# Kernel optimization log

Measured on AMD Instinct MI355X. Metric: run time of the kernel, lower is better.

Reference implementation:

```python
import jax, jax.numpy as jnp
import numpy as np

DIM = 784
HEADS = 2
DH = DIM // HEADS  # 392
EPS_LN = 1e-5
EPS_L2 = 1e-12


def layer_norm(x, w, b):
    mu = jnp.mean(x, axis=-1, keepdims=True)
    var = jnp.mean(jnp.square(x - mu), axis=-1, keepdims=True)
    return (x - mu) * jax.lax.rsqrt(var + EPS_LN) * w + b


def hardswish(x):
    return x * jnp.clip(x + 3.0, 0.0, 6.0) / 6.0


def l2norm(x):
    n = jnp.sqrt(jnp.sum(jnp.square(x), axis=-1, keepdims=True))
    return x / jnp.maximum(n, EPS_L2)


def setup_inputs() -> dict:
    key = jax.random.key(0)
    ks = jax.random.split(key, 8)
    B, N = 32, 1024
    x = jax.random.normal(ks[0], (B, N, DIM), dtype=jnp.float32)
    s = 0.02
    qkv_w = jax.random.normal(ks[1], (3 * DIM, DIM), dtype=jnp.float32) * s
    qkv_b = jax.random.normal(ks[2], (3 * DIM,), dtype=jnp.float32) * s
    out_w = jax.random.normal(ks[3], (DIM, DIM), dtype=jnp.float32) * s
    out_b = jax.random.normal(ks[4], (DIM,), dtype=jnp.float32) * s
    ffn_w = jax.random.normal(ks[5], (DIM, DIM), dtype=jnp.float32) * s
    ffn_b = jax.random.normal(ks[6], (DIM,), dtype=jnp.float32) * s
    ln_w = jnp.ones((DIM,), dtype=jnp.float32)
    ln_b = jnp.zeros((DIM,), dtype=jnp.float32)
    scale = jnp.ones((HEADS, 1, 1), dtype=jnp.float32) * 0.01
    return {"x": x, "ln_w": ln_w, "ln_b": ln_b, "qkv_w": qkv_w, "qkv_b": qkv_b,
            "scale": scale, "out_w": out_w, "out_b": out_b, "ffn_w": ffn_w, "ffn_b": ffn_b}


def reference(x, ln_w, ln_b, qkv_w, qkv_b, scale, out_w, out_b, ffn_w, ffn_b):
    B, N, _ = x.shape
    h = HEADS
    xn = layer_norm(x, ln_w, ln_b)
    qkv = xn @ qkv_w.T + qkv_b  # [B, N, 3*DIM]
    q, k, v = jnp.split(qkv, 3, axis=-1)
    # 'b n (h d) -> b h n d'
    def to_heads(t):
        return t.reshape(B, N, h, DH).transpose(0, 2, 1, 3)
    q, k, v = to_heads(q), to_heads(k), to_heads(v)
    q, k = l2norm(q), l2norm(k)
    sim = jnp.einsum('bhnd,bhmd->bhnm', q, k) * jnp.sqrt(scale)  # scale [h,1,1] broadcasts
    attn = jax.nn.softmax(sim, axis=-1)
    out = jnp.einsum('bhnm,bhmd->bhnd', attn, v)
    out = out.transpose(0, 2, 1, 3).reshape(B, N, DIM)  # 'b h n d -> b n (h d)'
    out = layer_norm(out, ln_w, ln_b)  # same LayerNorm params reused
    out = hardswish(out)
    out_ffn = hardswish(out @ ffn_w.T + ffn_b)
    return (out + out_ffn) @ out_w.T + out_b
```

## Files before the change

kernel.cpp:

```cpp
#include <hip/hip_runtime.h>

typedef unsigned short u16;
typedef unsigned int u32;
typedef __attribute__((ext_vector_type(4))) float f32x4;
typedef __attribute__((ext_vector_type(8))) short bf16x8;

#define TOK 32768
#define KP  832
#define DHP 448
#define DHPV 512
#define NQKV 2560

static __device__ __forceinline__ float bf2f(u16 u){ u32 v = ((u32)u)<<16; return __builtin_bit_cast(float, v); }
static __device__ __forceinline__ u16 f2bf(float f){
  u32 x = __builtin_bit_cast(u32, f);
  u32 r = (x + 0x7fffu + ((x>>16)&1u)) >> 16;
  return (u16)r;
}
static __device__ __forceinline__ void gload16(const void* g, void* l){
  __builtin_amdgcn_global_load_lds((const __attribute__((address_space(1))) void*)g,
                                   (__attribute__((address_space(3))) void*)l, 16, 0, 0);
}
static __device__ __forceinline__ float wave_red_sum(float v){
  #pragma unroll
  for (int o = 32; o > 0; o >>= 1) v += __shfl_xor(v, o, 64);
  return v;
}

__global__ __launch_bounds__(256) void wconv_k(const float* __restrict__ src, u16* __restrict__ dst,
                                               int srcR, long long total){
  long long i = (long long)blockIdx.x*256 + threadIdx.x;
  if (i >= total) return;
  int r = (int)(i / KP), c = (int)(i % KP);
  float v = (r < srcR && c < 784) ? src[(long long)r*784 + c] : 0.f;
  dst[i] = f2bf(v);
}

__global__ __launch_bounds__(256) void ln1_k(const float* __restrict__ x, const float* __restrict__ w,
                                             const float* __restrict__ b, u16* __restrict__ out){
  const int tid = threadIdx.x;
  const long long row = blockIdx.x;
  const float* xr = x + row*784;
  float v[4]; float s = 0.f, ss = 0.f;
  #pragma unroll
  for (int i = 0; i < 4; i++){ int c = tid + i*256; float t = (c < 784) ? xr[c] : 0.f; v[i] = t; s += t; ss += t*t; }
  __shared__ float red[8];
  s = wave_red_sum(s); ss = wave_red_sum(ss);
  if ((tid & 63) == 0){ red[tid>>6] = s; red[4 + (tid>>6)] = ss; }
  __syncthreads();
  float S  = red[0]+red[1]+red[2]+red[3];
  float SS = red[4]+red[5]+red[6]+red[7];
  float mean = S * (1.f/784.f);
  float var  = SS * (1.f/784.f) - mean*mean;
  float rstd = rsqrtf(var + 1e-5f);
  u16* orow = out + row*KP;
  #pragma unroll
  for (int i = 0; i < 4; i++){
    int c = tid + i*256;
    if (c < KP){
      u16 o = 0;
      if (c < 784) o = f2bf((v[i]-mean)*rstd*w[c] + b[c]);
      orow[c] = o;
    }
  }
}

__global__ __launch_bounds__(256) void ln2hs_k(const u16* __restrict__ a, const float* __restrict__ w,
                                               const float* __restrict__ b, u16* __restrict__ out){
  const int tid = threadIdx.x;
  const long long row = blockIdx.x;
  const u16* ar = a + row*784;
  float v[4]; float s = 0.f, ss = 0.f;
  #pragma unroll
  for (int i = 0; i < 4; i++){ int c = tid + i*256; float t = (c < 784) ? bf2f(ar[c]) : 0.f; v[i] = t; s += t; ss += t*t; }
  __shared__ float red[8];
  s = wave_red_sum(s); ss = wave_red_sum(ss);
  if ((tid & 63) == 0){ red[tid>>6] = s; red[4 + (tid>>6)] = ss; }
  __syncthreads();
  float S  = red[0]+red[1]+red[2]+red[3];
  float SS = red[4]+red[5]+red[6]+red[7];
  float mean = S * (1.f/784.f);
  float var  = SS * (1.f/784.f) - mean*mean;
  float rstd = rsqrtf(var + 1e-5f);
  u16* orow = out + row*KP;
  #pragma unroll
  for (int i = 0; i < 4; i++){
    int c = tid + i*256;
    if (c < KP){
      u16 o = 0;
      if (c < 784){
        float y = (v[i]-mean)*rstd*w[c] + b[c];
        y = y * fminf(fmaxf(y + 3.f, 0.f), 6.f) * (1.f/6.f);
        o = f2bf(y);
      }
      orow[c] = o;
    }
  }
}

__global__ __launch_bounds__(256) void l2n_k(u16* __restrict__ Q, u16* __restrict__ Kb,
                                             const float* __restrict__ scale){
  const int lane = threadIdx.x & 63, wv = threadIdx.x >> 6;
  const long long rid = (long long)blockIdx.x*4 + wv;
  const bool isK = rid >= 65536;
  const long long idx = isK ? rid - 65536 : rid;
  u16* base = (isK ? Kb : Q) + idx*DHP;
  uint2 t0 = *(const uint2*)(base + lane*4);
  int ch1 = lane + 64;
  uint2 t1 = (ch1 < 112) ? *(const uint2*)(base + ch1*4) : make_uint2(0u,0u);
  float f0[4], f1[4];
  u32 c0[2] = {t0.x, t0.y}, c1[2] = {t1.x, t1.y};
  #pragma unroll
  for (int j = 0; j < 4; j++){
    f0[j] = bf2f((u16)(c0[j>>1] >> ((j&1)*16)));
    f1[j] = bf2f((u16)(c1[j>>1] >> ((j&1)*16)));
  }
  float ssq = 0.f;
  #pragma unroll
  for (int j = 0; j < 4; j++) ssq += f0[j]*f0[j];
  if (ch1 < 98){
    #pragma unroll
    for (int j = 0; j < 4; j++) ssq += f1[j]*f1[j];
  }
  ssq = wave_red_sum(ssq);
  float fac = 1.f / fmaxf(sqrtf(ssq), 1e-12f);
  if (!isK) fac *= sqrtf(scale[(int)((idx >> 10) & 1)]);
  u32 o0[2], o1[2];
  #pragma unroll
  for (int j = 0; j < 2; j++){
    u16 lo = f2bf(f0[2*j]*fac),   hi = f2bf(f0[2*j+1]*fac);
    o0[j] = (u32)lo | ((u32)hi << 16);
    u16 lo1 = (ch1 < 98) ? f2bf(f1[2*j]*fac)   : (u16)0;
    u16 hi1 = (ch1 < 98) ? f2bf(f1[2*j+1]*fac) : (u16)0;
    o1[j] = (u32)lo1 | ((u32)hi1 << 16);
  }
  *(uint2*)(base + lane*4) = make_uint2(o0[0], o0[1]);
  if (ch1 < 112) *(uint2*)(base + ch1*4) = make_uint2(o1[0], o1[1]);
}

__global__ __launch_bounds__(512, 2) void attn_k(const u16* __restrict__ Qb, const u16* __restrict__ Kb,
    const u16* __restrict__ Vtb, u16* __restrict__ att)
{
  __shared__ u16 smem[32768];
  u16* Pbuf = smem + 16384;

  const int tid = threadIdx.x, lane = tid & 63, wid = tid >> 6;
  const int wq  = wid >> 2, kvw = wid & 3;
  const int dw  = wid >> 2, qw  = wid & 3;

  const int lin = (int)blockIdx.x;
  const int bh = (lin & 7)*8 + (lin >> 6);
  const int qt = (lin >> 3) & 7;

  const u16* Qp = Qb  + ((long long)bh*1024 + (long long)qt*128)*DHP;
  const u16* Kp = Kb  + (long long)bh*1024*DHP;
  const u16* Vp = Vtb + (long long)bh*DHPV*1024;

  const int srow = tid >> 2;
  const int scol = (((tid & 3) ^ ((srow >> 1) & 3)) << 3);
  const int s2   = tid + 512;
  const int r2   = s2 >> 2;
  const int c2   = (((s2 & 3) ^ ((r2 >> 1) & 3)) << 3);

  int offq[4], offk[2], offv[7];
  #pragma unroll
  for (int m = 0; m < 4; m++){
    int r = wq*64 + m*16 + (lane & 15);
    offq[m] = r*32 + ((((lane>>4) ^ (r>>1)) & 3) << 3);
  }
  #pragma unroll
  for (int n = 0; n < 2; n++){
    int r = kvw*32 + n*16 + (lane & 15);
    offk[n] = 4096 + r*32 + ((((lane>>4) ^ (r>>1)) & 3) << 3);
  }
  #pragma unroll
  for (int m = 0; m < 7; m++){
    int r = dw*112 + m*16 + (lane & 15);
    offv[m] = r*32 + ((((lane>>4) ^ (r>>1)) & 3) << 3);
  }

  auto stageA = [&](int ck, int t, int buf){
    u16* rb = smem + buf*8192;
    gload16(Qp + (long long)srow*DHP + t*32 + scol,            rb + tid*8);
    gload16(Kp + (long long)(ck*128 + srow)*DHP + t*32 + scol, rb + 4096 + tid*8);
  };
  auto stageV = [&](int ck, int ms, int buf){
    u16* rb = smem + buf*8192;
    const int h = ms >> 2, s = ms & 3;
    const u16* src = Vp + (long long)(h*224)*1024 + ck*128 + s*32;
    gload16(src + (long long)srow*1024 + scol, rb + tid*8);
    gload16(src + (long long)r2*1024  + c2,   rb + s2*8);
  };

  f32x4 oacc[2][7][2];
  #pragma unroll
  for (int h = 0; h < 2; h++)
    #pragma unroll
    for (int m = 0; m < 7; m++)
      #pragma unroll
      for (int n = 0; n < 2; n++) oacc[h][m][n] = f32x4{0.f,0.f,0.f,0.f};
  float rs_r[16];
  #pragma unroll
  for (int i = 0; i < 16; i++) rs_r[i] = 0.f;

  for (int ck = 0; ck < 8; ++ck){
    stageA(ck, 0, 0); stageA(ck, 1, 1);
    asm volatile("s_waitcnt vmcnt(2)" ::: "memory");
    __builtin_amdgcn_s_barrier();
    f32x4 sacc[4][2];
    #pragma unroll
    for (int m = 0; m < 4; m++)
      #pragma unroll
      for (int n = 0; n < 2; n++) sacc[m][n] = f32x4{0.f,0.f,0.f,0.f};

    for (int t = 0; t < 14; ++t){
      if (t + 2 < 14) stageA(ck, t+2, (t+2)%3);
      const u16* ra = smem + (t%3)*8192;
      bf16x8 aq[4], bk[2];
      #pragma unroll
      for (int m = 0; m < 4; m++) aq[m] = *(const bf16x8*)(ra + offq[m]);
      #pragma unroll
      for (int n = 0; n < 2; n++) bk[n] = *(const bf16x8*)(ra + offk[n]);
      __builtin_amdgcn_s_setprio(1);
      #pragma unroll
      for (int m = 0; m < 4; m++)
        #pragma unroll
        for (int n = 0; n < 2; n++)
          sacc[m][n] = __builtin_amdgcn_mfma_f32_16x16x32_bf16(aq[m], bk[n], sacc[m][n], 0, 0, 0);
      __builtin_amdgcn_s_setprio(0);
      if (t + 2 < 14)      asm volatile("s_waitcnt vmcnt(2)" ::: "memory");
      else if (t + 1 < 14) asm volatile("s_waitcnt vmcnt(0)" ::: "memory");
      if (t + 1 < 14) __builtin_amdgcn_s_barrier();
    }
    __builtin_amdgcn_s_barrier();

    stageV(ck, 0, 0);
    #pragma unroll
    for (int m = 0; m < 4; m++){
      #pragma unroll
      for (int i = 0; i < 4; i++){
        const int q = wq*64 + m*16 + (lane>>4)*4 + i;
        float a = 0.f;
        #pragma unroll
        for (int n = 0; n < 2; n++){
          const int kv = kvw*32 + n*16 + (lane & 15);
          u16 pb = f2bf(__expf(sacc[m][n][i]));
          Pbuf[q*128 + (((kv>>3) ^ (q&15)) << 3) + (kv&7)] = pb;
          a += bf2f(pb);
        }
        rs_r[m*4+i] += a;
      }
    }
    asm volatile("s_waitcnt vmcnt(0) lgkmcnt(0)" ::: "memory");
    __builtin_amdgcn_s_barrier();

    #pragma unroll
    for (int ms = 0; ms < 8; ++ms){
      if (ms + 1 < 8) stageV(ck, ms+1, (ms+1)&1);
      const u16* vb = smem + (ms&1)*8192;
      const int s = ms & 3;
      const int h = ms >> 2;
      bf16x8 av[7], bp[2];
      #pragma unroll
      for (int m = 0; m < 7; m++) av[m] = *(const bf16x8*)(vb + offv[m]);
      #pragma unroll
      for (int n = 0; n < 2; n++){
        const int q = qw*32 + n*16 + (lane & 15);
        const int cc = s*4 + (lane>>4);
        bp[n] = *(const bf16x8*)(Pbuf + q*128 + ((cc ^ (q&15)) << 3));
      }
      __builtin_amdgcn_s_setprio(1);
      #pragma unroll
      for (int m = 0; m < 7; m++)
        #pragma unroll
        for (int n = 0; n < 2; n++)
          oacc[h][m][n] = __builtin_amdgcn_mfma_f32_16x16x32_bf16(av[m], bp[n], oacc[h][m][n], 0, 0, 0);
      __builtin_amdgcn_s_setprio(0);
      if (ms + 1 < 8){
        asm volatile("s_waitcnt vmcnt(0)" ::: "memory");
        __builtin_amdgcn_s_barrier();
      }
    }
    __builtin_amdgcn_s_barrier();
  }

  float* rsL = (float*)&smem[0];
  float* rsT = rsL + 512;
  #pragma unroll
  for (int m = 0; m < 4; m++){
    #pragma unroll
    for (int i = 0; i < 4; i++){
      float v = rs_r[m*4+i];
      v += __shfl_xor(v, 1, 64); v += __shfl_xor(v, 2, 64);
      v += __shfl_xor(v, 4, 64); v += __shfl_xor(v, 8, 64);
      if ((lane & 15) == 0) rsL[(wq*64 + m*16 + (lane>>4)*4 + i)*4 + kvw] = v;
    }
  }
  __syncthreads();
  if (tid < 128) rsT[tid] = 1.f/(rsL[tid*4]+rsL[tid*4+1]+rsL[tid*4+2]+rsL[tid*4+3]);
  __syncthreads();
  const int b = bh >> 1, hh = bh & 1;
  #pragma unroll
  for (int h = 0; h < 2; h++){
    #pragma unroll
    for (int n = 0; n < 2; n++){
      const int q = qw*32 + n*16 + (lane & 15);
      const float rinv = rsT[q];
      u16* arw = att + ((long long)(b*1024 + qt*128 + q))*784 + hh*392;
      #pragma unroll
      for (int m = 0; m < 7; m++){
        const int d0 = h*224 + dw*112 + m*16 + (lane>>4)*4;
        if (d0 < 392){
          u16 a0 = f2bf(oacc[h][m][n][0]*rinv), a1 = f2bf(oacc[h][m][n][1]*rinv);
          u16 a2 = f2bf(oacc[h][m][n][2]*rinv), a3 = f2bf(oacc[h][m][n][3]*rinv);
          *(u32*)(arw + d0)     = (u32)a0 | ((u32)a1 << 16);
          *(u32*)(arw + d0 + 2) = (u32)a2 | ((u32)a3 << 16);
        }
      }
    }
  }
}

template<int EPI, int ORDER>
__global__ __launch_bounds__(512, 2) void gemm_k(const u16* __restrict__ Ab, const u16* __restrict__ Bb,
    int lda, int ldb, int nkt, long long sA, long long sB,
    const float* __restrict__ fp0, void* __restrict__ vp1, void* __restrict__ vp2, void* __restrict__ vp3)
{
  __shared__ u16 LA[3][8192];
  __shared__ u16 LB[3][4096];
  const int tid = threadIdx.x;
  const int lane = tid & 63;
  const int wid = tid >> 6;
  const int wr = wid >> 1, wc = wid & 1;

  const int gx = gridDim.x, gy = gridDim.y;
  const int nwg = gx*gy;
  int lin = (ORDER == 0) ? ((int)blockIdx.x + gx*(int)blockIdx.y)
                         : ((int)blockIdx.y + gy*(int)blockIdx.x);
  const int q8 = nwg >> 3, r8 = nwg & 7;
  const int xcd = lin & 7, base8 = lin >> 3;
  int wg = (xcd < r8 ? xcd*(q8+1) : r8*(q8+1) + (xcd-r8)*q8) + base8;
  int bx, by;
  if (ORDER == 0){ bx = wg % gx; by = wg / gx; }
  else           { by = wg % gy; bx = wg / gy; }

  const u16* A  = Ab + (long long)by*256*lda;
  const u16* Bp = Bb + (long long)bx*128*ldb;

  const int s0 = tid, s1 = tid + 512;
  const int r0 = s0 >> 2, r1 = s1 >> 2;
  const int kc0 = (((s0 & 3) ^ ((s0 >> 3) & 3)) << 3);
  const int kc1 = (((s1 & 3) ^ ((s1 >> 3) & 3)) << 3);
  const u16* ga0 = A  + (long long)r0*lda + kc0;
  const u16* ga1 = A  + (long long)r1*lda + kc1;
  const u16* gb0 = Bp + (long long)r0*ldb + kc0;

  int offa[4], offb[4];
  #pragma unroll
  for (int m = 0; m < 4; m++){
    int row = wr*64 + m*16 + (lane & 15);
    offa[m] = row*32 + ((((lane >> 4) ^ (row >> 1)) & 3) << 3);
  }
  #pragma unroll
  for (int n = 0; n < 4; n++){
    int row = wc*64 + n*16 + (lane & 15);
    offb[n] = row*32 + ((((lane >> 4) ^ (row >> 1)) & 3) << 3);
  }

  f32x4 acc[4][4];
  #pragma unroll
  for (int m = 0; m < 4; m++)
    #pragma unroll
    for (int n = 0; n < 4; n++) acc[m][n] = f32x4{0.f,0.f,0.f,0.f};

  auto stage = [&](int tt){
    const int b = tt % 3;
    const long long k0 = (long long)(tt << 5);
    gload16(ga0 + k0, (void*)&LA[b][s0*8]);
    gload16(ga1 + k0, (void*)&LA[b][s1*8]);
    gload16(gb0 + k0, (void*)&LB[b][tid*8]);
  };

  stage(0); stage(1);
  asm volatile("s_waitcnt vmcnt(3)" ::: "memory");
  __builtin_amdgcn_s_barrier();

  for (int t = 0; t < nkt; ++t){
    if (t + 2 < nkt) stage(t + 2);
    const int b = t % 3;
    bf16x8 af[4], bf[4];
    #pragma unroll
    for (int m = 0; m < 4; m++) af[m] = *(const bf16x8*)&LA[b][offa[m]];
    #pragma unroll
    for (int n = 0; n < 4; n++) bf[n] = *(const bf16x8*)&LB[b][offb[n]];
    __builtin_amdgcn_s_setprio(1);
    #pragma unroll
    for (int m = 0; m < 4; m++)
      #pragma unroll
      for (int n = 0; n < 4; n++)
        acc[m][n] = __builtin_amdgcn_mfma_f32_16x16x32_bf16(af[m], bf[n], acc[m][n], 0, 0, 0);
    __builtin_amdgcn_s_setprio(0);
    if (t + 2 < nkt)      asm volatile("s_waitcnt vmcnt(3)" ::: "memory");
    else if (t + 1 < nkt) asm volatile("s_waitcnt vmcnt(0)" ::: "memory");
    if (t + 1 < nkt) __builtin_amdgcn_s_barrier();
  }

  const int tm = by*256 + wr*64;
  const int tn = bx*128 + wc*64;

  if constexpr (EPI == 0){
    u16* Qn = (u16*)vp1; u16* Kn = (u16*)vp2; u16* Vt = (u16*)vp3;
    #pragma unroll
    for (int m = 0; m < 4; m++){
      const int row0 = tm + m*16 + (lane>>4)*4;
      if (row0 < 2352){
        const int seg = row0 / 392;
        const int hh = seg & 1;
        const int dd0 = row0 - seg*392;
        const float b0 = fp0[row0], b1 = fp0[row0+1], b2 = fp0[row0+2], b3 = fp0[row0+3];
        #pragma unroll
        for (int n = 0; n < 4; n++){
          const int col = tn + n*16 + (lane&15);
          const int bb = col >> 10, nn = col & 1023;
          if (seg < 4){
            u16* dst = (seg < 2) ? Qn : Kn;
            ushort4 pk;
            pk.x = f2bf(acc[m][n][0] + b0);
            pk.y = f2bf(acc[m][n][1] + b1);
            pk.z = f2bf(acc[m][n][2] + b2);
            pk.w = f2bf(acc[m][n][3] + b3);
            *(ushort4*)(dst + ((long long)((bb*2 + hh)*1024 + nn))*DHP + dd0) = pk;
          } else {
            const long long vb = ((long long)(bb*2 + hh)*DHPV + dd0)*1024 + nn;
            Vt[vb        ] = f2bf(acc[m][n][0] + b0);
            Vt[vb + 1024 ] = f2bf(acc[m][n][1] + b1);
            Vt[vb + 2048 ] = f2bf(acc[m][n][2] + b2);
            Vt[vb + 3072 ] = f2bf(acc[m][n][3] + b3);
          }
        }
      }
    }
  } else {
    #pragma unroll
    for (int m = 0; m < 4; m++){
      #pragma unroll
      for (int n = 0; n < 4; n++){
        #pragma unroll
        for (int i = 0; i < 4; i++){
          const int row = tm + m*16 + (lane>>4)*4 + i;
          const int col = tn + n*16 + (lane&15);
          float v = acc[m][n][i];
          if constexpr (EPI == 4){
            if (col < KP){
              u16 o = 0;
              if (col < 784){
                float f = v + fp0[col];
                f = f * fminf(fmaxf(f + 3.f, 0.f), 6.f) * (1.f/6.f);
                float hv = bf2f(((const u16*)vp1)[(long long)row*KP + col]);
                o = f2bf(hv + f);
              }
              ((u16*)vp2)[(long long)row*KP + col] = o;
            }
          } else {
            if (col < 784){
              ((float*)vp1)[(long long)row*784 + col] = v + fp0[col];
            }
          }
        }
      }
    }
  }
}

extern "C" void kernel_launch(void* const* d_in, const int* in_sizes, int n_in,
                              void* d_out, int out_size, void* d_ws, size_t ws_size,
                              hipStream_t stream)
{
  const float* x     = (const float*)d_in[0];
  const float* ln_w  = (const float*)d_in[1];
  const float* ln_b  = (const float*)d_in[2];
  const float* qkv_w = (const float*)d_in[3];
  const float* qkv_b = (const float*)d_in[4];
  const float* scale = (const float*)d_in[5];
  const float* out_w = (const float*)d_in[6];
  const float* out_b = (const float*)d_in[7];
  const float* ffn_w = (const float*)d_in[8];
  const float* ffn_b = (const float*)d_in[9];

  char* wsp = (char*)d_ws;
  auto alloc = [&](long long bytes)->char*{ char* p = wsp; wsp += (bytes + 255) & ~255LL; return p; };
  u16* XN   = (u16*)alloc((long long)TOK*KP*2);
  u16* WQKV = (u16*)alloc((long long)NQKV*KP*2);
  u16* WFF  = (u16*)alloc(1024LL*KP*2);
  u16* WO   = (u16*)alloc(1024LL*KP*2);
  u16* QN   = (u16*)alloc(64LL*1024*DHP*2);
  u16* KN   = (u16*)alloc(64LL*1024*DHP*2);
  u16* VT   = (u16*)alloc(64LL*DHPV*1024*2);
  u16* ATT = XN;
  u16* H   = QN;
  u16* S   = KN;
  (void)ws_size; (void)in_sizes; (void)n_in; (void)out_size;

  wconv_k<<<dim3(((long long)NQKV*KP + 255)/256), 256, 0, stream>>>(qkv_w, WQKV, 2352, (long long)NQKV*KP);
  wconv_k<<<dim3((1024*KP + 255)/256), 256, 0, stream>>>(ffn_w, WFF, 784, 1024LL*KP);
  wconv_k<<<dim3((1024*KP + 255)/256), 256, 0, stream>>>(out_w, WO,  784, 1024LL*KP);

  ln1_k<<<dim3(TOK), 256, 0, stream>>>(x, ln_w, ln_b, XN);
  gemm_k<0,1><<<dim3(256, 10, 1), 512, 0, stream>>>(WQKV, XN, KP, KP, 26, 0LL, 0LL,
      qkv_b, QN, KN, VT);
  l2n_k<<<dim3(32768), 256, 0, stream>>>(QN, KN, scale);
  attn_k<<<dim3(512), 512, 0, stream>>>(QN, KN, VT, ATT);
  ln2hs_k<<<dim3(TOK), 256, 0, stream>>>(ATT, ln_w, ln_b, H);
  gemm_k<4,0><<<dim3(7, 128, 1), 512, 0, stream>>>(H, WFF, KP, KP, 26, 0LL, 0LL, ffn_b, H, S, nullptr);
  gemm_k<5,0><<<dim3(7, 128, 1), 512, 0, stream>>>(S, WO, KP, KP, 26, 0LL, 0LL, out_b, d_out, nullptr, nullptr);
}
```

Measured before the change: 714.8 us.

## Triple-buffer V staging in attention and restructure GEMM K-loop into paired half-tiles

The attention kernel now prefetches V two stages ahead with a three-slot ring buffer instead of double buffering, waiting on vmcnt(2) so loads overlap with more MFMA work. The GEMM kernel merges the A and B shared buffers into four 24KB slots and processes K in 64-wide steps split into two halves, prefetching the next step's halves while computing the current ones. The GEMM swizzle also changes from (s>>3)&3 to (row>>1)&3. Shared memory rises to 80KB in attention and 96KB in the GEMM, which at two blocks per CU may limit occupancy.

```diff
diff --git a/kernel.cpp b/kernel.cpp
--- a/kernel.cpp
+++ b/kernel.cpp
@@ -141,8 +141,8 @@
 __global__ __launch_bounds__(512, 2) void attn_k(const u16* __restrict__ Qb, const u16* __restrict__ Kb,
     const u16* __restrict__ Vtb, u16* __restrict__ att)
 {
-  __shared__ u16 smem[32768];
-  u16* Pbuf = smem + 16384;
+  __shared__ u16 smem[40960];
+  u16* Pbuf = smem + 24576;
 
   const int tid = threadIdx.x, lane = tid & 63, wid = tid >> 6;
   const int wq  = wid >> 2, kvw = wid & 3;
@@ -234,7 +234,7 @@
     }
     __builtin_amdgcn_s_barrier();
 
-    stageV(ck, 0, 0);
+    stageV(ck, 0, 0); stageV(ck, 1, 1);
     #pragma unroll
     for (int m = 0; m < 4; m++){
       #pragma unroll
@@ -251,13 +251,13 @@
         rs_r[m*4+i] += a;
       }
     }
-    asm volatile("s_waitcnt vmcnt(0) lgkmcnt(0)" ::: "memory");
+    asm volatile("s_waitcnt vmcnt(2) lgkmcnt(0)" ::: "memory");
     __builtin_amdgcn_s_barrier();
 
     #pragma unroll
     for (int ms = 0; ms < 8; ++ms){
-      if (ms + 1 < 8) stageV(ck, ms+1, (ms+1)&1);
-      const u16* vb = smem + (ms&1)*8192;
+      if (ms + 2 < 8) stageV(ck, ms+2, (ms+2)%3);
+      const u16* vb = smem + (ms%3)*8192;
       const int s = ms & 3;
       const int h = ms >> 2;
       bf16x8 av[7], bp[2];
@@ -276,10 +276,9 @@
         for (int n = 0; n < 2; n++)
           oacc[h][m][n] = __builtin_amdgcn_mfma_f32_16x16x32_bf16(av[m], bp[n], oacc[h][m][n], 0, 0, 0);
       __builtin_amdgcn_s_setprio(0);
-      if (ms + 1 < 8){
-        asm volatile("s_waitcnt vmcnt(0)" ::: "memory");
-        __builtin_amdgcn_s_barrier();
-      }
+      if (ms + 2 < 8)      asm volatile("s_waitcnt vmcnt(2)" ::: "memory");
+      else if (ms + 1 < 8) asm volatile("s_waitcnt vmcnt(0)" ::: "memory");
+      if (ms + 1 < 8) __builtin_amdgcn_s_barrier();
     }
     __builtin_amdgcn_s_barrier();
   }
@@ -326,8 +325,7 @@
     int lda, int ldb, int nkt, long long sA, long long sB,
     const float* __restrict__ fp0, void* __restrict__ vp1, void* __restrict__ vp2, void* __restrict__ vp3)
 {
-  __shared__ u16 LA[3][8192];
-  __shared__ u16 LB[3][4096];
+  __shared__ u16 L[4][12288];
   const int tid = threadIdx.x;
   const int lane = tid & 63;
   const int wid = tid >> 6;
@@ -347,13 +345,22 @@
   const u16* A  = Ab + (long long)by*256*lda;
   const u16* Bp = Bb + (long long)bx*128*ldb;
 
-  const int s0 = tid, s1 = tid + 512;
-  const int r0 = s0 >> 2, r1 = s1 >> 2;
-  const int kc0 = (((s0 & 3) ^ ((s0 >> 3) & 3)) << 3);
-  const int kc1 = (((s1 & 3) ^ ((s1 >> 3) & 3)) << 3);
-  const u16* ga0 = A  + (long long)r0*lda + kc0;
-  const u16* ga1 = A  + (long long)r1*lda + kc1;
-  const u16* gb0 = Bp + (long long)r0*ldb + kc0;
+  const int ra0 = tid >> 2;
+  const int ka0 = ((((tid) & 3) ^ ((ra0 >> 1) & 3)) << 3);
+  const int ra1 = (tid + 512) >> 2;
+  const int ka1 = ((((tid + 512) & 3) ^ ((ra1 >> 1) & 3)) << 3);
+  const u16* gA0 = A  + (long long)ra0*lda + ka0;
+  const u16* gA1 = A  + (long long)ra1*lda + ka1;
+  const u16* gB0 = Bp + (long long)ra0*ldb + ka0;
+
+  auto stage = [&](int t, int h){
+    const int hb = ((t & 1) << 1) | h;
+    u16* dst = &L[hb][0];
+    const int k0 = (t << 6) + (h << 5);
+    gload16(gA0 + k0, dst + tid*8);
+    gload16(gA1 + k0, dst + (tid + 512)*8);
+    gload16(gB0 + k0, dst + 8192 + tid*8);
+  };
 
   int offa[4], offb[4];
   #pragma unroll
@@ -364,7 +371,7 @@
   #pragma unroll
   for (int n = 0; n < 4; n++){
     int row = wc*64 + n*16 + (lane & 15);
-    offb[n] = row*32 + ((((lane >> 4) ^ (row >> 1)) & 3) << 3);
+    offb[n] = 8192 + row*32 + ((((lane >> 4) ^ (row >> 1)) & 3) << 3);
   }
 
   f32x4 acc[4][4];
@@ -373,36 +380,32 @@
     #pragma unroll
     for (int n = 0; n < 4; n++) acc[m][n] = f32x4{0.f,0.f,0.f,0.f};
 
-  auto stage = [&](int tt){
-    const int b = tt % 3;
-    const long long k0 = (long long)(tt << 5);
-    gload16(ga0 + k0, (void*)&LA[b][s0*8]);
-    gload16(ga1 + k0, (void*)&LA[b][s1*8]);
-    gload16(gb0 + k0, (void*)&LB[b][tid*8]);
-  };
-
-  stage(0); stage(1);
+  stage(0, 0); stage(0, 1);
   asm volatile("s_waitcnt vmcnt(3)" ::: "memory");
   __builtin_amdgcn_s_barrier();
 
   for (int t = 0; t < nkt; ++t){
-    if (t + 2 < nkt) stage(t + 2);
-    const int b = t % 3;
-    bf16x8 af[4], bf[4];
-    #pragma unroll
-    for (int m = 0; m < 4; m++) af[m] = *(const bf16x8*)&LA[b][offa[m]];
-    #pragma unroll
-    for (int n = 0; n < 4; n++) bf[n] = *(const bf16x8*)&LB[b][offb[n]];
-    __builtin_amdgcn_s_setprio(1);
-    #pragma unroll
-    for (int m = 0; m < 4; m++)
-      #pragma unroll
-      for (int n = 0; n < 4; n++)
-        acc[m][n] = __builtin_amdgcn_mfma_f32_16x16x32_bf16(af[m], bf[n], acc[m][n], 0, 0, 0);
-    __builtin_amdgcn_s_setprio(0);
-    if (t + 2 < nkt)      asm volatile("s_waitcnt vmcnt(3)" ::: "memory");
-    else if (t + 1 < nkt) asm volatile("s_waitcnt vmcnt(0)" ::: "memory");
-    if (t + 1 < nkt) __builtin_amdgcn_s_barrier();
+    const bool lastT = (t == nkt - 1);
+    #pragma unroll
+    for (int h = 0; h < 2; ++h){
+      if (!lastT) stage(t + 1, h);
+      const int hb = ((t & 1) << 1) | h;
+      bf16x8 af[4], bf[4];
+      #pragma unroll
+      for (int m = 0; m < 4; m++) af[m] = *(const bf16x8*)&L[hb][offa[m]];
+      #pragma unroll
+      for (int n = 0; n < 4; n++) bf[n] = *(const bf16x8*)&L[hb][offb[n]];
+      __builtin_amdgcn_s_setprio(1);
+      #pragma unroll
+      for (int m = 0; m < 4; m++)
+        #pragma unroll
+        for (int n = 0; n < 4; n++)
+          acc[m][n] = __builtin_amdgcn_mfma_f32_16x16x32_bf16(af[m], bf[n], acc[m][n], 0, 0, 0);
+      __builtin_amdgcn_s_setprio(0);
+      if (!lastT)          asm volatile("s_waitcnt vmcnt(3)" ::: "memory");
+      else if (h == 0)     asm volatile("s_waitcnt vmcnt(0)" ::: "memory");
+      if (!(lastT && h == 1)) __builtin_amdgcn_s_barrier();
+    }
   }
 
   const int tm = by*256 + wr*64;
@@ -506,11 +509,11 @@
   wconv_k<<<dim3((1024*KP + 255)/256), 256, 0, stream>>>(out_w, WO,  784, 1024LL*KP);
 
   ln1_k<<<dim3(TOK), 256, 0, stream>>>(x, ln_w, ln_b, XN);
-  gemm_k<0,1><<<dim3(256, 10, 1), 512, 0, stream>>>(WQKV, XN, KP, KP, 26, 0LL, 0LL,
+  gemm_k<0,1><<<dim3(256, 10, 1), 512, 0, stream>>>(WQKV, XN, KP, KP, 13, 0LL, 0LL,
       qkv_b, QN, KN, VT);
   l2n_k<<<dim3(32768), 256, 0, stream>>>(QN, KN, scale);
   attn_k<<<dim3(512), 512, 0, stream>>>(QN, KN, VT, ATT);
   ln2hs_k<<<dim3(TOK), 256, 0, stream>>>(ATT, ln_w, ln_b, H);
-  gemm_k<4,0><<<dim3(7, 128, 1), 512, 0, stream>>>(H, WFF, KP, KP, 26, 0LL, 0LL, ffn_b, H, S, nullptr);
-  gemm_k<5,0><<<dim3(7, 128, 1), 512, 0, stream>>>(S, WO, KP, KP, 26, 0LL, 0LL, out_b, d_out, nullptr, nullptr);
-}
+  gemm_k<4,0><<<dim3(7, 128, 1), 512, 0, stream>>>(H, WFF, KP, KP, 13, 0LL, 0LL, ffn_b, H, S, nullptr);
+  gemm_k<5,0><<<dim3(7, 128, 1), 512, 0, stream>>>(S, WO, KP, KP, 13, 0LL, 0LL, out_b, d_out, nullptr, nullptr);
+}
```

Result: no change. 719.6 us (+0.7%).
